# Optimization experiments

Measured on AMD Instinct MI355X. Metric: run time of the kernel, lower is better.

## Reference

```python
import jax, jax.numpy as jnp
import numpy as np

N = 100000   # nodes
E = 1000000  # edges
DS = 16      # stage start/end scale-out vec dim
DC = 224     # raw context dim
CC = DS + DC + DS  # context_channels = 256
DM = 128     # stage_metrics_channels
H = (CC + DM) // 2  # 192 hidden of final_transform
OUT = 128    # out_channels (== DM, required by overwrite path)


def setup_inputs() -> dict:
    key = jax.random.key(0)
    ks = jax.random.split(key, 16)
    n = lambda k, shape, s=0.05: jax.random.normal(k, shape, jnp.float32) * s
    return {
        "edge_index": jax.random.randint(ks[0], (2, E), 0, N, dtype=jnp.int64),
        "stage_start": jax.random.normal(ks[1], (N, DS), jnp.float32),
        "stage_end": jax.random.normal(ks[2], (N, DS), jnp.float32),
        "context": jax.random.normal(ks[3], (N, DC), jnp.float32),
        "stage_metrics": jax.random.normal(ks[4], (N, DM), jnp.float32),
        "W_l": n(ks[5], (CC, CC)), "b_l": jnp.zeros((CC,), jnp.float32),
        "W_r": n(ks[6], (CC, CC)), "b_r": jnp.zeros((CC,), jnp.float32),
        "att": n(ks[7], (CC,)),
        "W1": n(ks[8], (CC + DM, H)), "b1": jnp.zeros((H,), jnp.float32),
        "W2": n(ks[9], (H, OUT)), "b2": jnp.zeros((OUT,), jnp.float32),
        "bias": jnp.zeros((OUT,), jnp.float32),
    }


def reference(edge_index, stage_start, stage_end, context, stage_metrics,
              W_l, b_l, W_r, b_r, att, W1, b1, W2, b2, bias):
    # node transform: [N, CC]
    nc = jnp.concatenate([stage_start, context, stage_end], axis=-1)
    cl = nc @ W_l + b_l  # source-side (j)
    cr = nc @ W_r + b_r  # target-side (i)

    src, dst = edge_index[0], edge_index[1]  # flow: source_to_target, aggregate by dst
    ci = cr[dst]                 # [E, CC] context_i
    cj = cl[src]                 # [E, CC] context_j
    mj = stage_metrics[src]      # [E, DM] metrics_j

    ctx = jax.nn.selu(ci + cj)
    ctx = jnp.where(jnp.all(mj == 0, axis=1, keepdims=True), 0.0, ctx)

    alpha = ctx @ att            # [E]
    mask = alpha != 0            # ~zero_indices

    # segment softmax over non-zero alphas, grouped by dst (PyG softmax: sub max, exp, /sum+eps)
    NEG = jnp.float32(-1e30)
    m = jax.ops.segment_max(jnp.where(mask, alpha, NEG), dst, num_segments=N)
    ex = jnp.where(mask, jnp.exp(alpha - m[dst]), 0.0)
    s = jax.ops.segment_sum(ex, dst, num_segments=N)
    a = jnp.where(mask, ex / (s[dst] + 1e-16), 0.0)

    # per-edge 2-layer SELU MLP
    h = jax.nn.selu(jnp.concatenate([ctx, mj], axis=-1) @ W1 + b1)  # [E, H]
    f = jax.nn.selu(h @ W2 + b2)                                    # [E, OUT]
    msg = jnp.where(mask[:, None], f * a[:, None], 0.0)

    # scatter-add aggregation to nodes
    out = jax.ops.segment_sum(msg, dst, num_segments=N)  # [N, OUT]

    # rows with all-zero aggregation are overwritten by stage_metrics; others get bias + sigmoid
    ovr = jnp.all(out == 0, axis=1, keepdims=True)
    return jnp.where(ovr, stage_metrics, jax.nn.sigmoid(out + bias))
```

## Files before the change

### kernel.cpp

```cpp
#include <hip/hip_runtime.h>
#include <hip/hip_bf16.h>
#include <math.h>

#define NN   100000
#define EE   1000000
#define CCH  256
#define DMC  128
#define HDC  192
#define OUTC 128
#define ET   32
#define MS   132
#define GS   391

typedef unsigned short u16;
using bf16x8 = __attribute__((ext_vector_type(8))) short;
using f32x4  = __attribute__((ext_vector_type(4))) float;
using u16x4  = __attribute__((ext_vector_type(4))) unsigned short;
using u16x8  = __attribute__((ext_vector_type(8))) unsigned short;

__device__ __forceinline__ float selu_f(float x) {
    const float sc = 1.0507009873554804934193349852946f;
    const float c1 = 1.7580993408473765792727863477367f;
    const float e = __expf(x);
    return x > 0.0f ? sc * x : __builtin_fmaf(c1, e, -c1);
}
__device__ __forceinline__ u16 f2bf(float f) {
    union { __hip_bfloat16 h; u16 u; } c;
    c.h = __float2bfloat16(f);
    return c.u;
}
__device__ __forceinline__ float bf2f(u16 h) {
    return __uint_as_float(((unsigned int)h) << 16);
}

__global__ __launch_bounds__(256, 2) void k_node_gemm(
    const float* __restrict__ ss, const float* __restrict__ se,
    const float* __restrict__ ctx, const u16* __restrict__ W0p,
    const float* __restrict__ bl, const float* __restrict__ br,
    u16* __restrict__ clb, u16* __restrict__ crb)
{
    __shared__ __align__(16) char Xs[64 * 512];
    const int tid = threadIdx.x;
    const int wave = tid >> 6, lane = tid & 63;
    const int node0 = blockIdx.x * 64;

    {
        const int r = lane;
        const int nd = min(node0 + r, NN - 1);
#pragma unroll
        for (int i = 0; i < 8; ++i) {
            const int c0 = wave * 64 + i * 8;
            float4 va, vb;
            {
                const int c = c0;
                if (c < 16)       va = *reinterpret_cast<const float4*>(ss + nd * 16 + c);
                else if (c < 240) va = *reinterpret_cast<const float4*>(ctx + (size_t)nd * 224 + (c - 16));
                else              va = *reinterpret_cast<const float4*>(se + nd * 16 + (c - 240));
            }
            {
                const int c = c0 + 4;
                if (c < 16)       vb = *reinterpret_cast<const float4*>(ss + nd * 16 + c);
                else if (c < 240) vb = *reinterpret_cast<const float4*>(ctx + (size_t)nd * 224 + (c - 16));
                else              vb = *reinterpret_cast<const float4*>(se + nd * 16 + (c - 240));
            }
            u16x8 v;
            v[0] = f2bf(va.x); v[1] = f2bf(va.y); v[2] = f2bf(va.z); v[3] = f2bf(va.w);
            v[4] = f2bf(vb.x); v[5] = f2bf(vb.y); v[6] = f2bf(vb.z); v[7] = f2bf(vb.w);
            *reinterpret_cast<u16x8*>(Xs + r * 512 + ((c0 * 2) ^ ((r & 7) << 4))) = v;
        }
    }
    __syncthreads();

    const int r16   = lane & 15;
    const int khalf = (lane >> 4) << 4;
    const int rbase = (lane >> 4) * 4;

    f32x4 acc[4][8];
#pragma unroll
    for (int m = 0; m < 4; ++m)
#pragma unroll
        for (int jj = 0; jj < 8; ++jj) acc[m][jj] = (f32x4){0.f, 0.f, 0.f, 0.f};

    for (int ks = 0; ks < 8; ++ks) {
        bf16x8 b[8];
#pragma unroll
        for (int jj = 0; jj < 8; ++jj)
            b[jj] = *reinterpret_cast<const bf16x8*>(
                W0p + (((size_t)(wave + 4 * jj) * 8 + ks) * 64 + lane) * 8);
        const int kb = ks * 64 + khalf;
#pragma unroll
        for (int m = 0; m < 4; ++m) {
            const int row = m * 16 + r16;
            const bf16x8 a = *reinterpret_cast<const bf16x8*>(
                Xs + row * 512 + (kb ^ ((row & 7) << 4)));
#pragma unroll
            for (int jj = 0; jj < 8; ++jj)
                acc[m][jj] = __builtin_amdgcn_mfma_f32_16x16x32_bf16(a, b[jj], acc[m][jj], 0, 0, 0);
        }
    }

#pragma unroll
    for (int jj = 0; jj < 8; ++jj) {
        const int nt = wave + 4 * jj;
        const bool isL = nt < 16;
        const int ncl = (isL ? nt * 16 : (nt - 16) * 16) + r16;
        const float bias = isL ? bl[ncl] : br[ncl];
        u16* base = (isL ? clb : crb) + ncl;
#pragma unroll
        for (int m = 0; m < 4; ++m)
#pragma unroll
            for (int rr = 0; rr < 4; ++rr) {
                const int node = node0 + m * 16 + rbase + rr;
                if (node < NN)
                    base[(size_t)node * CCH] = f2bf(acc[m][jj][rr] + bias);
            }
    }
}

__global__ __launch_bounds__(256) void k_convert(
    const float* __restrict__ in, u16* __restrict__ out, int n)
{
    const int i = (blockIdx.x * 256 + threadIdx.x) * 4;
    if (i < n) {
        const float4 v = *reinterpret_cast<const float4*>(in + i);
        u16x4 o; o[0] = f2bf(v.x); o[1] = f2bf(v.y); o[2] = f2bf(v.z); o[3] = f2bf(v.w);
        *reinterpret_cast<u16x4*>(out + i) = o;
    }
}

__global__ __launch_bounds__(64) void k_pack_w(
    const float* __restrict__ W, u16* __restrict__ out, int K, int N)
{
    const int f = blockIdx.x, lane = threadIdx.x;
    const int KS = K >> 5;
    const int nt = f / KS, ks = f - nt * KS;
    const int n = nt * 16 + (lane & 15);
    const int k0 = ks * 32 + (lane >> 4) * 8;
    u16x8 v;
#pragma unroll
    for (int j = 0; j < 8; ++j) v[j] = f2bf(W[(size_t)(k0 + j) * N + n]);
    *reinterpret_cast<u16x8*>(out + ((size_t)f * 64 + lane) * 8) = v;
}

__global__ __launch_bounds__(64) void k_pack_att(
    const float* __restrict__ att, u16* __restrict__ attp)
{
    const int ks = blockIdx.x;
    const int lane = threadIdx.x;
    const int nloc = lane & 15;
    const int k0 = ks * 32 + (lane >> 4) * 8;
    u16x8 v;
#pragma unroll
    for (int j = 0; j < 8; ++j) v[j] = f2bf((nloc == 0) ? att[k0 + j] : 0.f);
    *reinterpret_cast<u16x8*>(attp + ((size_t)ks * 64 + lane) * 8) = v;
}

__global__ __launch_bounds__(256) void k_hist(
    const int* __restrict__ ei, int* __restrict__ cnt)
{
    const int i = blockIdx.x * 256 + threadIdx.x;
    if (i < EE / 4) {
        const int4 d = *reinterpret_cast<const int4*>(ei + EE + i * 4);
        atomicAdd(&cnt[d.x], 1); atomicAdd(&cnt[d.y], 1);
        atomicAdd(&cnt[d.z], 1); atomicAdd(&cnt[d.w], 1);
    }
}

__global__ __launch_bounds__(256) void k_scan1(
    const int* __restrict__ cnt, int* __restrict__ bsum)
{
    const int i = blockIdx.x * 256 + threadIdx.x;
    int v = (i < NN) ? cnt[i] : 0;
#pragma unroll
    for (int o = 1; o < 64; o <<= 1) v += __shfl_xor(v, o);
    __shared__ int ws[4];
    if ((threadIdx.x & 63) == 0) ws[threadIdx.x >> 6] = v;
    __syncthreads();
    if (threadIdx.x == 0) bsum[blockIdx.x] = ws[0] + ws[1] + ws[2] + ws[3];
}

__global__ __launch_bounds__(512) void k_scan2(int* __restrict__ bsum)
{
    __shared__ int s[512];
    const int t = threadIdx.x;
    const int v = (t < GS) ? bsum[t] : 0;
    s[t] = v;
    __syncthreads();
    for (int o = 1; o < 512; o <<= 1) {
        const int u = (t >= o) ? s[t - o] : 0;
        __syncthreads();
        s[t] += u;
        __syncthreads();
    }
    if (t < GS) bsum[t] = s[t] - v;
}

__global__ __launch_bounds__(256) void k_scan3(
    const int* __restrict__ cnt, const int* __restrict__ bsum,
    int* __restrict__ cur)
{
    const int t = threadIdx.x;
    const int i = blockIdx.x * 256 + t;
    const int lane = t & 63, w = t >> 6;
    const int v = (i < NN) ? cnt[i] : 0;
    int x = v;
#pragma unroll
    for (int o = 1; o < 64; o <<= 1) {
        const int u = __shfl_up(x, o);
        if (lane >= o) x += u;
    }
    __shared__ int wsum[4];
    if (lane == 63) wsum[w] = x;
    __syncthreads();
    int off = bsum[blockIdx.x];
    for (int k2 = 0; k2 < w; ++k2) off += wsum[k2];
    if (i < NN) cur[i] = off + x - v;
}

__global__ __launch_bounds__(256) void k_scatter(
    const int* __restrict__ ei, int* __restrict__ cur, int* __restrict__ perm)
{
    const int i = blockIdx.x * 256 + threadIdx.x;
    if (i < EE) {
        const int d = ei[EE + i];
        const int pos = atomicAdd(&cur[d], 1);
        perm[pos] = i;
    }
}

__global__ __launch_bounds__(256, 6) void k_edge_mlp(
    const int* __restrict__ ei, const int* __restrict__ perm,
    const u16* __restrict__ clb, const u16* __restrict__ crb,
    const u16* __restrict__ metb, const u16* __restrict__ attp,
    float* __restrict__ sb,
    const u16* __restrict__ W1p, const float* __restrict__ b1,
    const u16* __restrict__ W2p, const float* __restrict__ b2,
    float* __restrict__ dout)
{
    __shared__ __align__(16) char Xs[ET * 768];
    __shared__ int esrc[ET], edst[ET], flg[ET];
    __shared__ float exs[ET];

    const int tid  = threadIdx.x;
    const int wave = tid >> 6;
    const int lane = tid & 63;
    const int ebase = blockIdx.x * ET;

    if (tid < ET) {
        const int e = perm[ebase + tid];
        esrc[tid] = ei[e];
        edst[tid] = ei[EE + e];
        flg[tid] = 0;
    }
    __syncthreads();

#pragma unroll
    for (int i = 0; i < ET * 48 / 256; ++i) {
        const int k = tid + i * 256;
        const int t = k / 48, c = k - t * 48;
        u16x8 v;
        if (c < 32) {
            const u16x8 r = *reinterpret_cast<const u16x8*>(crb + (size_t)edst[t] * CCH + c * 8);
            const u16x8 l = *reinterpret_cast<const u16x8*>(clb + (size_t)esrc[t] * CCH + c * 8);
#pragma unroll
            for (int j = 0; j < 8; ++j) v[j] = f2bf(selu_f(bf2f(r[j]) + bf2f(l[j])));
        } else {
            v = *reinterpret_cast<const u16x8*>(metb + (size_t)esrc[t] * DMC + (c - 32) * 8);
            unsigned ob = 0;
#pragma unroll
            for (int j = 0; j < 8; ++j) ob |= (unsigned)v[j];
            if (ob & 0x7fffu) atomicOr(&flg[t], 1);
        }
        *reinterpret_cast<u16x8*>(Xs + t * 768 + ((c * 16) ^ ((t & 7) << 4))) = v;
    }
    __syncthreads();

    const int r16   = lane & 15;
    const int khalf = (lane >> 4) << 4;
    const int rbase = (lane >> 4) * 4;

    f32x4 acc[2][3];
    f32x4 acc3[2];
#pragma unroll
    for (int m = 0; m < 2; ++m) {
#pragma unroll
        for (int j = 0; j < 3; ++j) acc[m][j] = (f32x4){0.f, 0.f, 0.f, 0.f};
        acc3[m] = (f32x4){0.f, 0.f, 0.f, 0.f};
    }

    for (int ks = 0; ks < 12; ++ks) {
        bf16x8 b[3];
#pragma unroll
        for (int j = 0; j < 3; ++j)
            b[j] = *reinterpret_cast<const bf16x8*>(
                W1p + (((size_t)(wave + 4 * j) * 12 + ks) * 64 + lane) * 8);
        bf16x8 b3 = {};
        const bool doA = (wave == 0) && (ks < 8);
        if (doA)
            b3 = *reinterpret_cast<const bf16x8*>(attp + ((size_t)ks * 64 + lane) * 8);
        const int kb = ks * 64 + khalf;
#pragma unroll
        for (int m = 0; m < 2; ++m) {
            const int row = m * 16 + r16;
            const bf16x8 a = *reinterpret_cast<const bf16x8*>(
                Xs + row * 768 + (kb ^ ((row & 7) << 4)));
#pragma unroll
            for (int j = 0; j < 3; ++j)
                acc[m][j] = __builtin_amdgcn_mfma_f32_16x16x32_bf16(a, b[j], acc[m][j], 0, 0, 0);
            if (doA)
                acc3[m] = __builtin_amdgcn_mfma_f32_16x16x32_bf16(a, b3, acc3[m], 0, 0, 0);
        }
    }

    if (wave == 0 && r16 == 0) {
        const int hi = lane >> 4;
#pragma unroll
        for (int m = 0; m < 2; ++m)
#pragma unroll
            for (int r = 0; r < 4; ++r) {
                const int e = m * 16 + hi * 4 + r;
                const float al = acc3[m][r];
                exs[e] = (flg[e] && al != 0.f) ? __expf(al) : 0.f;
            }
    }
    __syncthreads();

#pragma unroll
    for (int j = 0; j < 3; ++j) {
        const int n = (wave + 4 * j) * 16 + r16;
        const float bb = b1[n];
#pragma unroll
        for (int m = 0; m < 2; ++m)
#pragma unroll
            for (int r = 0; r < 4; ++r) {
                const int row = m * 16 + rbase + r;
                *reinterpret_cast<u16*>(Xs + row * 384 + ((n * 2) ^ ((row & 7) << 4))) =
                    f2bf(selu_f(acc[m][j][r] + bb));
            }
    }
    __syncthreads();

    f32x4 acc2[2][2];
#pragma unroll
    for (int m = 0; m < 2; ++m)
#pragma unroll
        for (int j = 0; j < 2; ++j) acc2[m][j] = (f32x4){0.f, 0.f, 0.f, 0.f};

    for (int ks = 0; ks < 6; ++ks) {
        bf16x8 b[2];
#pragma unroll
        for (int j = 0; j < 2; ++j)
            b[j] = *reinterpret_cast<const bf16x8*>(
                W2p + (((size_t)(wave + 4 * j) * 6 + ks) * 64 + lane) * 8);
        const int kb = ks * 64 + khalf;
#pragma unroll
        for (int m = 0; m < 2; ++m) {
            const int row = m * 16 + r16;
            const bf16x8 a = *reinterpret_cast<const bf16x8*>(
                Xs + row * 384 + (kb ^ ((row & 7) << 4)));
#pragma unroll
            for (int j = 0; j < 2; ++j)
                acc2[m][j] = __builtin_amdgcn_mfma_f32_16x16x32_bf16(a, b[j], acc2[m][j], 0, 0, 0);
        }
    }
    __syncthreads();

    float* Ms = (float*)Xs;
#pragma unroll
    for (int j = 0; j < 2; ++j) {
        const int n = (wave + 4 * j) * 16 + r16;
        const float bb = b2[n];
#pragma unroll
        for (int m = 0; m < 2; ++m)
#pragma unroll
            for (int r = 0; r < 4; ++r) {
                const int e = m * 16 + rbase + r;
                Ms[e * MS + n] = selu_f(acc2[m][j][r] + bb) * exs[e];
            }
    }
    if (tid < ET) Ms[tid * MS + 128] = exs[tid];
    __syncthreads();

    {
        const int col = tid & 127;
        const int h = tid >> 7;
        const int r0 = h * 16;
        int cur_d = edst[r0];
        float s = Ms[r0 * MS + col];
        for (int r = r0 + 1; r < r0 + 16; ++r) {
            const int d = edst[r];
            const float v = Ms[r * MS + col];
            if (d != cur_d) {
                if (s != 0.f) atomicAdd(&dout[(size_t)cur_d * OUTC + col], s);
                cur_d = d; s = v;
            } else {
                s += v;
            }
        }
        if (s != 0.f) atomicAdd(&dout[(size_t)cur_d * OUTC + col], s);
    }
    if (tid < 2) {
        const int r0 = tid * 16;
        int cur_d = edst[r0];
        float s = Ms[r0 * MS + 128];
        for (int r = r0 + 1; r < r0 + 16; ++r) {
            const int d = edst[r];
            const float v = Ms[r * MS + 128];
            if (d != cur_d) {
                if (s != 0.f) atomicAdd(&sb[cur_d], s);
                cur_d = d; s = v;
            } else {
                s += v;
            }
        }
        if (s != 0.f) atomicAdd(&sb[cur_d], s);
    }
}

__global__ __launch_bounds__(64) void k_finalize(
    float* __restrict__ dout, const float* __restrict__ met,
    const float* __restrict__ bias, const float* __restrict__ sb)
{
    const int n = blockIdx.x;
    const int lane = threadIdx.x;
    const float a0 = dout[(size_t)n * OUTC + lane];
    const float a1 = dout[(size_t)n * OUTC + 64 + lane];
    const bool ovr = __all((a0 == 0.f) && (a1 == 0.f));
    float r0, r1;
    if (ovr) {
        r0 = met[(size_t)n * DMC + lane];
        r1 = met[(size_t)n * DMC + 64 + lane];
    } else {
        const float inv = 1.0f / (sb[n] + 1e-16f);
        r0 = 1.f / (1.f + __expf(-(a0 * inv + bias[lane])));
        r1 = 1.f / (1.f + __expf(-(a1 * inv + bias[64 + lane])));
    }
    dout[(size_t)n * OUTC + lane] = r0;
    dout[(size_t)n * OUTC + 64 + lane] = r1;
}

extern "C" void kernel_launch(void* const* d_in, const int* in_sizes, int n_in,
                              void* d_out, int out_size, void* d_ws, size_t ws_size,
                              hipStream_t stream)
{
    const int*   ei   = (const int*)d_in[0];
    const float* ss   = (const float*)d_in[1];
    const float* se   = (const float*)d_in[2];
    const float* ctx  = (const float*)d_in[3];
    const float* met  = (const float*)d_in[4];
    const float* Wl   = (const float*)d_in[5];
    const float* bl   = (const float*)d_in[6];
    const float* Wr   = (const float*)d_in[7];
    const float* br   = (const float*)d_in[8];
    const float* att  = (const float*)d_in[9];
    const float* W1   = (const float*)d_in[10];
    const float* b1   = (const float*)d_in[11];
    const float* W2   = (const float*)d_in[12];
    const float* b2   = (const float*)d_in[13];
    const float* bias = (const float*)d_in[14];

    u16* clb  = (u16*)d_ws;
    u16* crb  = clb  + (size_t)NN * CCH;
    u16* metb = crb  + (size_t)NN * CCH;
    u16* W1p  = metb + (size_t)NN * DMC;
    u16* W2p  = W1p  + (size_t)(CCH + DMC) * HDC;
    u16* W0p  = W2p  + (size_t)HDC * OUTC;
    float* sb = (float*)(W0p + (size_t)CCH * 512);
    int* cnt  = (int*)(sb + NN);
    int* cur  = cnt + NN;
    int* perm = cur + NN;
    int* bsum = perm + EE;
    u16* attp = (u16*)(bsum + 512);

    float* dout = (float*)d_out;

    hipMemsetAsync(dout, 0, (size_t)NN * OUTC * sizeof(float), stream);
    hipMemsetAsync(sb, 0, (size_t)NN * sizeof(float), stream);
    hipMemsetAsync(cnt, 0, (size_t)NN * sizeof(int), stream);

    k_hist<<<(EE / 4 + 255) / 256, 256, 0, stream>>>(ei, cnt);
    k_scan1<<<GS, 256, 0, stream>>>(cnt, bsum);
    k_scan2<<<1, 512, 0, stream>>>(bsum);
    k_scan3<<<GS, 256, 0, stream>>>(cnt, bsum, cur);
    k_scatter<<<(EE + 255) / 256, 256, 0, stream>>>(ei, cur, perm);

    k_pack_w<<<(CCH / 16) * (CCH / 32), 64, 0, stream>>>(Wl, W0p, CCH, CCH);
    k_pack_w<<<(CCH / 16) * (CCH / 32), 64, 0, stream>>>(Wr, W0p + (size_t)128 * 64 * 8, CCH, CCH);
    k_pack_w<<<(HDC / 16) * ((CCH + DMC) / 32), 64, 0, stream>>>(W1, W1p, CCH + DMC, HDC);
    k_pack_w<<<(OUTC / 16) * (HDC / 32), 64, 0, stream>>>(W2, W2p, HDC, OUTC);
    k_pack_att<<<8, 64, 0, stream>>>(att, attp);
    k_convert<<<(NN * DMC / 4 + 255) / 256, 256, 0, stream>>>(met, metb, NN * DMC);

    k_node_gemm<<<(NN + 63) / 64, 256, 0, stream>>>(ss, se, ctx, W0p, bl, br, clb, crb);
    k_edge_mlp<<<EE / ET, 256, 0, stream>>>(ei, perm, clb, crb, metb, attp, sb,
                                            W1p, b1, W2p, b2, dout);
    k_finalize<<<NN, 64, 0, stream>>>(dout, met, bias, sb);
}
```

Before: 787.6 us.

## Store sorted src/dst directly, batch gather loads, widen finalize blocks

The scatter step now writes the sorted source and destination indices directly, replacing a permutation array, so the edge kernel no longer makes a dependent indirect read of edge_index. The edge kernel issues all its gather loads up front before doing the SELU math, which exposes more memory-level parallelism. It also replaces the shared-memory atomicOr for the zero-metrics flag with a wave ballot. Finalize now packs four nodes into each 256-thread block. The cost is an extra 4MB index array in the workspace and more registers held by the prefetched vectors.

```diff
diff --git a/kernel.cpp b/kernel.cpp
--- a/kernel.cpp
+++ b/kernel.cpp
@@ -218,18 +218,20 @@
 }
 
 __global__ __launch_bounds__(256) void k_scatter(
-    const int* __restrict__ ei, int* __restrict__ cur, int* __restrict__ perm)
+    const int* __restrict__ ei, int* __restrict__ cur,
+    int* __restrict__ srcs, int* __restrict__ dsts)
 {
     const int i = blockIdx.x * 256 + threadIdx.x;
     if (i < EE) {
         const int d = ei[EE + i];
         const int pos = atomicAdd(&cur[d], 1);
-        perm[pos] = i;
+        srcs[pos] = ei[i];
+        dsts[pos] = d;
     }
 }
 
 __global__ __launch_bounds__(256, 6) void k_edge_mlp(
-    const int* __restrict__ ei, const int* __restrict__ perm,
+    const int* __restrict__ srcs, const int* __restrict__ dsts,
     const u16* __restrict__ clb, const u16* __restrict__ crb,
     const u16* __restrict__ metb, const u16* __restrict__ attp,
     float* __restrict__ sb,
@@ -247,31 +249,45 @@
     const int ebase = blockIdx.x * ET;
 
     if (tid < ET) {
-        const int e = perm[ebase + tid];
-        esrc[tid] = ei[e];
-        edst[tid] = ei[EE + e];
-        flg[tid] = 0;
-    }
-    __syncthreads();
-
-#pragma unroll
-    for (int i = 0; i < ET * 48 / 256; ++i) {
+        esrc[tid] = srcs[ebase + tid];
+        edst[tid] = dsts[ebase + tid];
+    }
+    __syncthreads();
+
+    u16x8 rv[4], lv[4], mv[2];
+#pragma unroll
+    for (int i = 0; i < 4; ++i) {
         const int k = tid + i * 256;
-        const int t = k / 48, c = k - t * 48;
+        const int t = k >> 5, c = k & 31;
+        rv[i] = *reinterpret_cast<const u16x8*>(crb + (size_t)edst[t] * CCH + c * 8);
+        lv[i] = *reinterpret_cast<const u16x8*>(clb + (size_t)esrc[t] * CCH + c * 8);
+    }
+#pragma unroll
+    for (int i = 0; i < 2; ++i) {
+        const int k = tid + i * 256;
+        mv[i] = *reinterpret_cast<const u16x8*>(metb + (size_t)esrc[k >> 4] * DMC + (k & 15) * 8);
+    }
+#pragma unroll
+    for (int i = 0; i < 4; ++i) {
+        const int k = tid + i * 256;
+        const int t = k >> 5, c = k & 31;
         u16x8 v;
-        if (c < 32) {
-            const u16x8 r = *reinterpret_cast<const u16x8*>(crb + (size_t)edst[t] * CCH + c * 8);
-            const u16x8 l = *reinterpret_cast<const u16x8*>(clb + (size_t)esrc[t] * CCH + c * 8);
-#pragma unroll
-            for (int j = 0; j < 8; ++j) v[j] = f2bf(selu_f(bf2f(r[j]) + bf2f(l[j])));
-        } else {
-            v = *reinterpret_cast<const u16x8*>(metb + (size_t)esrc[t] * DMC + (c - 32) * 8);
-            unsigned ob = 0;
-#pragma unroll
-            for (int j = 0; j < 8; ++j) ob |= (unsigned)v[j];
-            if (ob & 0x7fffu) atomicOr(&flg[t], 1);
-        }
+#pragma unroll
+        for (int j = 0; j < 8; ++j) v[j] = f2bf(selu_f(bf2f(rv[i][j]) + bf2f(lv[i][j])));
         *reinterpret_cast<u16x8*>(Xs + t * 768 + ((c * 16) ^ ((t & 7) << 4))) = v;
+    }
+#pragma unroll
+    for (int i = 0; i < 2; ++i) {
+        const int k = tid + i * 256;
+        const int t = k >> 4, g = k & 15;
+        unsigned ob = 0;
+#pragma unroll
+        for (int j = 0; j < 8; ++j) ob |= (unsigned)mv[i][j];
+        const bool nz = (ob & 0x7fffu) != 0u;
+        const unsigned long long bal = __ballot(nz);
+        if ((lane & 15) == 0)
+            flg[t] = (int)((bal >> ((lane >> 4) * 16)) & 0xFFFFull) != 0;
+        *reinterpret_cast<u16x8*>(Xs + t * 768 + (((32 + g) * 16) ^ ((t & 7) << 4))) = mv[i];
     }
     __syncthreads();
 
@@ -417,12 +433,12 @@
     }
 }
 
-__global__ __launch_bounds__(64) void k_finalize(
+__global__ __launch_bounds__(256) void k_finalize(
     float* __restrict__ dout, const float* __restrict__ met,
     const float* __restrict__ bias, const float* __restrict__ sb)
 {
-    const int n = blockIdx.x;
-    const int lane = threadIdx.x;
+    const int n = blockIdx.x * 4 + (threadIdx.x >> 6);
+    const int lane = threadIdx.x & 63;
     const float a0 = dout[(size_t)n * OUTC + lane];
     const float a1 = dout[(size_t)n * OUTC + 64 + lane];
     const bool ovr = __all((a0 == 0.f) && (a1 == 0.f));
@@ -468,8 +484,9 @@
     float* sb = (float*)(W0p + (size_t)CCH * 512);
     int* cnt  = (int*)(sb + NN);
     int* cur  = cnt + NN;
-    int* perm = cur + NN;
-    int* bsum = perm + EE;
+    int* srcs = cur + NN;
+    int* dsts = srcs + EE;
+    int* bsum = dsts + EE;
     u16* attp = (u16*)(bsum + 512);
 
     float* dout = (float*)d_out;
@@ -482,7 +499,7 @@
     k_scan1<<<GS, 256, 0, stream>>>(cnt, bsum);
     k_scan2<<<1, 512, 0, stream>>>(bsum);
     k_scan3<<<GS, 256, 0, stream>>>(cnt, bsum, cur);
-    k_scatter<<<(EE + 255) / 256, 256, 0, stream>>>(ei, cur, perm);
+    k_scatter<<<(EE + 255) / 256, 256, 0, stream>>>(ei, cur, srcs, dsts);
 
     k_pack_w<<<(CCH / 16) * (CCH / 32), 64, 0, stream>>>(Wl, W0p, CCH, CCH);
     k_pack_w<<<(CCH / 16) * (CCH / 32), 64, 0, stream>>>(Wr, W0p + (size_t)128 * 64 * 8, CCH, CCH);
@@ -492,7 +509,7 @@
     k_convert<<<(NN * DMC / 4 + 255) / 256, 256, 0, stream>>>(met, metb, NN * DMC);
 
     k_node_gemm<<<(NN + 63) / 64, 256, 0, stream>>>(ss, se, ctx, W0p, bl, br, clb, crb);
-    k_edge_mlp<<<EE / ET, 256, 0, stream>>>(ei, perm, clb, crb, metb, attp, sb,
+    k_edge_mlp<<<EE / ET, 256, 0, stream>>>(srcs, dsts, clb, crb, metb, attp, sb,
                                             W1p, b1, W2p, b2, dout);
-    k_finalize<<<NN, 64, 0, stream>>>(dout, met, bias, sb);
-}
+    k_finalize<<<NN / 4, 256, 0, stream>>>(dout, met, bias, sb);
+}
```

Result: faster. 706.0 us (-10.4%).
